# Kernel optimization log

Measured on AMD Instinct MI355X. Metric: run time of the kernel, lower is better.

The kernel has to match this reference:

```python
import math
import jax, jax.numpy as jnp
import numpy as np

B, S, D, H = 2, 2048, 2048, 16
HD = D // H
INV_NORM = 1.0 / math.sqrt(HD)


def _build_alibi(batch, n_heads, seq_len):
    # Standard BLOOM ALiBi slopes (n_heads is a power of two here)
    base = 2.0 ** (-(2.0 ** -(math.log2(n_heads) - 3)))
    slopes = base ** np.arange(1, n_heads + 1, dtype=np.float32)  # [H]
    pos = np.arange(seq_len, dtype=np.float32)  # [S]
    alibi = slopes[:, None] * pos[None, :]  # [H, S]
    alibi = np.broadcast_to(alibi[None], (batch, n_heads, seq_len)).reshape(batch * n_heads, 1, seq_len)
    return jnp.asarray(alibi)


def _build_causal_mask(batch, seq_len):
    neg = jnp.float32(-1e9)
    tril = jnp.tril(jnp.ones((seq_len, seq_len), dtype=bool))
    mask = jnp.where(tril, jnp.float32(0.0), neg)  # [S, S]
    return jnp.broadcast_to(mask[None, None], (batch, 1, seq_len, seq_len))


def setup_inputs() -> dict:
    key = jax.random.key(0)
    ks = jax.random.split(key, 6)
    scale = 0.02
    return {
        "hidden_states": jax.random.normal(ks[0], (B, S, D), jnp.float32),
        "residual": jax.random.normal(ks[1], (B, S, D), jnp.float32),
        "alibi": _build_alibi(B, H, S),
        "attention_mask": _build_causal_mask(B, S),
        "W_qkv": jax.random.normal(ks[2], (3 * D, D), jnp.float32) * scale,
        "b_qkv": jax.random.normal(ks[3], (3 * D,), jnp.float32) * scale,
        "W_dense": jax.random.normal(ks[4], (D, D), jnp.float32) * scale,
        "b_dense": jax.random.normal(ks[5], (D,), jnp.float32) * scale,
    }


def reference(hidden_states, residual, alibi, attention_mask, W_qkv, b_qkv, W_dense, b_dense):
    b, s, d = hidden_states.shape
    # fused QKV projection: [B,S,3D] -> [B,S,H,3,HD]
    fused = (hidden_states @ W_qkv.T + b_qkv).reshape(b, s, H, 3, HD)
    q = fused[..., 0, :].transpose(0, 2, 1, 3)  # [B,H,S,HD]
    k = fused[..., 1, :].transpose(0, 2, 1, 3)
    v = fused[..., 2, :].transpose(0, 2, 1, 3)
    # baddbmm: alibi + inv_norm * q @ k^T ; alibi is [B*H,1,S] -> broadcast over q_len
    scores = alibi.reshape(b, H, 1, s) + INV_NORM * jnp.einsum("bhqd,bhkd->bhqk", q, k)
    scores = scores + attention_mask  # additive causal mask [B,1,S,S]
    probs = jax.nn.softmax(scores.astype(jnp.float32), axis=-1).astype(hidden_states.dtype)
    ctx = jnp.einsum("bhqk,bhkd->bhqd", probs, v)  # [B,H,S,HD]
    ctx = ctx.transpose(0, 2, 1, 3).reshape(b, s, d)  # merge heads
    out = ctx @ W_dense.T + b_dense
    return out + residual  # dropout_add with p=0 (eval)
```

## Files before the change

kernel.cpp:

```cpp
#include <hip/hip_runtime.h>
#include <hip/hip_bf16.h>

typedef __hip_bfloat16 bf16;
typedef __attribute__((ext_vector_type(8))) short s8v;
typedef __attribute__((ext_vector_type(4))) float f4v;

#define B_  2
#define S_  2048
#define D_  2048
#define H_  16
#define HD_ 128
#define INV_NORM 0.08838834764831845f

static __device__ __forceinline__ f4v mfma16(s8v a, s8v b, f4v c) {
    return __builtin_amdgcn_mfma_f32_16x16x32_bf16(a, b, c, 0, 0, 0);
}

static __device__ __forceinline__ void gload_lds(const void* gp, void* lp) {
    __builtin_amdgcn_global_load_lds(
        (const __attribute__((address_space(1))) unsigned int*)gp,
        (__attribute__((address_space(3))) unsigned int*)lp, 16, 0, 0);
}

__global__ __launch_bounds__(256)
void cvt_f32_bf16(const float* __restrict__ src, bf16* __restrict__ dst, int n4)
{
    int i = blockIdx.x * 256 + threadIdx.x;
    if (i < n4) {
        float4 f = ((const float4*)src)[i];
        union { ushort4 u4; bf16 h[4]; } p;
        p.h[0] = __float2bfloat16(f.x);
        p.h[1] = __float2bfloat16(f.y);
        p.h[2] = __float2bfloat16(f.z);
        p.h[3] = __float2bfloat16(f.w);
        ((ushort4*)dst)[i] = p.u4;
    }
}

template <int MODE>
__global__ __launch_bounds__(256)
void gemm_bt(const bf16* __restrict__ A, const bf16* __restrict__ Bw,
             const float* __restrict__ bias, const float* __restrict__ resid,
             bf16* __restrict__ o0, bf16* __restrict__ o1, bf16* __restrict__ o2,
             float* __restrict__ of, int K)
{
    __shared__ __align__(16) bf16 Al[128][32];
    __shared__ __align__(16) bf16 Bl[128][32];
    const int tid  = threadIdx.x;
    const int wave = tid >> 6, lane = tid & 63;
    const int col  = lane & 15, quad = lane >> 4;
    const int wm = (wave >> 1) << 6, wn = (wave & 1) << 6;
    const int bn = blockIdx.x, bm = blockIdx.y;
    const bf16* Ab = A  + (size_t)bm * 128 * K;
    const bf16* Bb = Bw + (size_t)bn * 128 * K;

    const f4v fzero = {0.f, 0.f, 0.f, 0.f};
    f4v acc[4][4];
#pragma unroll
    for (int i = 0; i < 4; i++)
#pragma unroll
        for (int j = 0; j < 4; j++) acc[i][j] = fzero;

    for (int k0 = 0; k0 < K; k0 += 32) {
#pragma unroll
        for (int p = 0; p < 2; p++) {
            const int g = p * 256 + tid;
            const int r = g >> 2, ko = (g & 3) << 3;
            gload_lds(Ab + (size_t)r * K + k0 + ko, (char*)&Al[0][0] + (size_t)g * 16);
            gload_lds(Bb + (size_t)r * K + k0 + ko, (char*)&Bl[0][0] + (size_t)g * 16);
        }
        __syncthreads();
        s8v af[4], bfr[4];
#pragma unroll
        for (int i = 0; i < 4; i++) af[i]  = *(const s8v*)&Al[wm + i * 16 + col][quad * 8];
#pragma unroll
        for (int j = 0; j < 4; j++) bfr[j] = *(const s8v*)&Bl[wn + j * 16 + col][quad * 8];
#pragma unroll
        for (int i = 0; i < 4; i++)
#pragma unroll
            for (int j = 0; j < 4; j++)
                acc[i][j] = mfma16(af[i], bfr[j], acc[i][j]);
        __syncthreads();
    }

    if (MODE == 0) {
        const int t = bn % 3, h = bn / 3;
#pragma unroll
        for (int j = 0; j < 4; j++) {
            const int c = wn + j * 16 + col;
            const float bv = bias[bn * 128 + c];
#pragma unroll
            for (int i = 0; i < 4; i++) {
                const int r  = (bm << 7) + wm + i * 16 + (quad << 2);
                const int bb = r >> 11, s = r & (S_ - 1);
                if (t == 2) {
                    union { ushort4 u4; bf16 hh[4]; } pk;
#pragma unroll
                    for (int rg = 0; rg < 4; rg++)
                        pk.hh[rg] = __float2bfloat16(acc[i][j][rg] + bv);
                    *(ushort4*)(o2 + ((size_t)(bb * H_ + h) * HD_ + c) * S_ + s) = pk.u4;
                } else {
                    bf16* dst = (t == 0) ? o0 : o1;
#pragma unroll
                    for (int rg = 0; rg < 4; rg++)
                        dst[((size_t)(bb * H_ + h) * S_ + (s + rg)) * HD_ + c] =
                            __float2bfloat16(acc[i][j][rg] + bv);
                }
            }
        }
    } else {
#pragma unroll
        for (int j = 0; j < 4; j++) {
            const int c = (bn << 7) + wn + j * 16 + col;
            const float bv = bias[c];
#pragma unroll
            for (int i = 0; i < 4; i++) {
                const int r = (bm << 7) + wm + i * 16 + (quad << 2);
#pragma unroll
                for (int rg = 0; rg < 4; rg++) {
                    const size_t idx = (size_t)(r + rg) * D_ + c;
                    of[idx] = acc[i][j][rg] + bv + resid[idx];
                }
            }
        }
    }
}

#define VMW(s) asm volatile("s_waitcnt " s ::: "memory")
#define BARR() { __builtin_amdgcn_s_barrier(); asm volatile("" ::: "memory"); }

#define RD_A(dst, mibase)                                                       \
  _Pragma("unroll") for (int mi = 0; mi < 4; ++mi) {                            \
    dst[mi][0] = *(const s8v*)(lds + bufB + aR + (mibase + mi) * 4096 + sx0);   \
    dst[mi][1] = *(const s8v*)(lds + bufB + aR + (mibase + mi) * 4096 + sx1);   \
  }
#define RD_B(njbase)                                                            \
  _Pragma("unroll") for (int nj = 0; nj < 2; ++nj) {                            \
    bfr[nj][0] = *(const s8v*)(lds + bufB + bRo + (njbase + nj) * 8192 + sx0);  \
    bfr[nj][1] = *(const s8v*)(lds + bufB + bRo + (njbase + nj) * 8192 + sx1);  \
  }
#define MM(af, mibase, njbase)                                                  \
  __builtin_amdgcn_s_setprio(1);                                                \
  _Pragma("unroll") for (int mi = 0; mi < 4; ++mi)                              \
  _Pragma("unroll") for (int nj = 0; nj < 2; ++nj) {                            \
    acc[mibase + mi][njbase + nj] =                                             \
        mfma16(af[mi][0], bfr[nj][0], acc[mibase + mi][njbase + nj]);           \
    acc[mibase + mi][njbase + nj] =                                             \
        mfma16(af[mi][1], bfr[nj][1], acc[mibase + mi][njbase + nj]);           \
  }                                                                             \
  __builtin_amdgcn_s_setprio(0);

#define KTILE(DOPRE, VA, VB, VC)                                                \
  {                                                                             \
    const int bufB = cur << 16, bufN = (cur ^ 1) << 16;                         \
    const size_t t1 = (size_t)(kt + 1) * 64;                                    \
                          \
    if (DOPRE) { gload_lds(gA + t1 + srcO0, lds + bufN + 0 + dst0);             \
                 gload_lds(gA + t1 + srcO1, lds + bufN + 0 + dst1); }           \
    VMW(VA); BARR();                                                            \
    RD_A(a0, 0); RD_B(0);                                                       \
    MM(a0, 0, 0);                                                               \
                               \
    if (DOPRE) { gload_lds(gB + t1 + srcO0, lds + bufN + 32768 + dst0);         \
                 gload_lds(gB + t1 + srcO1, lds + bufN + 32768 + dst1); }       \
    VMW(VB); BARR();                                                            \
    RD_A(a1, 4);                                                                \
    MM(a1, 4, 0);                                                               \
                               \
    if (DOPRE) { gload_lds(gA2 + t1 + srcO0, lds + bufN + 16384 + dst0);        \
                 gload_lds(gA2 + t1 + srcO1, lds + bufN + 16384 + dst1); }      \
    VMW(VC); BARR();                                                            \
    RD_B(2);                                                                    \
    MM(a0, 0, 2);                                                               \
    BARR();     \
                         \
    if (DOPRE) { gload_lds(gB2 + t1 + srcO0, lds + bufN + 49152 + dst0);        \
                 gload_lds(gB2 + t1 + srcO1, lds + bufN + 49152 + dst1); }      \
    MM(a1, 4, 2);                                                               \
  }

__global__ __launch_bounds__(512, 2)
void gemm_qkv8(const bf16* __restrict__ A, const bf16* __restrict__ Bw,
               const float* __restrict__ bias,
               bf16* __restrict__ o0, bf16* __restrict__ o1, bf16* __restrict__ o2)
{
    __shared__ __align__(16) char lds[131072];
    const int tid  = threadIdx.x;
    const int wave = tid >> 6, lane = tid & 63;
    const int col  = lane & 15, quad = lane >> 4;
    const int wr   = wave >> 2, wc = wave & 3;

    int id = (int)blockIdx.y * 24 + (int)blockIdx.x;
    id = (id & 7) * 48 + (id >> 3);
    const int bm = id / 24, bn = id % 24;

    const bf16* gA  = A  + (size_t)bm * 256 * 2048;
    const bf16* gA2 = gA + (size_t)128 * 2048;
    const bf16* gB  = Bw + (size_t)bn * 256 * 2048;
    const bf16* gB2 = gB + (size_t)128 * 2048;

    const int r0   = tid >> 3, bk0 = tid & 7;
    const int srcO0 = r0 * 2048 + ((bk0 ^ (r0 & 7)) << 3);
    const int srcO1 = srcO0 + 64 * 2048;
    const int dst0 = tid * 16, dst1 = dst0 + 8192;

    const int sx0 = ((quad ^ (col & 7)) << 4);
    const int sx1 = (((4 + quad) ^ (col & 7)) << 4);
    const int aR  = (wr * 16 + col) * 128;
    const int bRo = (wc * 16 + col) * 128 + 32768;

    const f4v fzero = {0.f, 0.f, 0.f, 0.f};
    f4v acc[8][4];
#pragma unroll
    for (int i = 0; i < 8; i++)
#pragma unroll
        for (int j = 0; j < 4; j++) acc[i][j] = fzero;
    s8v a0[4][2], a1[4][2], bfr[2][2];

    gload_lds(gA  + srcO0, lds + 0     + dst0);
    gload_lds(gA  + srcO1, lds + 0     + dst1);
    gload_lds(gB  + srcO0, lds + 32768 + dst0);
    gload_lds(gB  + srcO1, lds + 32768 + dst1);
    gload_lds(gA2 + srcO0, lds + 16384 + dst0);
    gload_lds(gA2 + srcO1, lds + 16384 + dst1);
    gload_lds(gB2 + srcO0, lds + 49152 + dst0);
    gload_lds(gB2 + srcO1, lds + 49152 + dst1);

    int cur = 0;
    for (int kt = 0; kt < 31; ++kt) {
        KTILE(1, "vmcnt(6)", "vmcnt(6)", "vmcnt(6)");
        cur ^= 1;
    }
    {
        const int kt = 31;
        KTILE(0, "vmcnt(4)", "vmcnt(2)", "vmcnt(0)");
    }

#pragma unroll
    for (int mi = 0; mi < 8; ++mi) {
#pragma unroll
        for (int nj = 0; nj < 4; ++nj) {
            const int cg = bn * 2 + (nj >> 1);
            const int t3 = cg % 3, hh = cg / 3;
            const int hd = (nj & 1) * 64 + wc * 16 + col;
            const float bv = bias[cg * 128 + hd];
            const int r = bm * 256 + mi * 32 + wr * 16 + (quad << 2);
            const int bi = r >> 11, srow = r & (S_ - 1);
            if (t3 == 2) {
                union { ushort4 u4; bf16 hv[4]; } pk;
#pragma unroll
                for (int rg = 0; rg < 4; ++rg)
                    pk.hv[rg] = __float2bfloat16(acc[mi][nj][rg] + bv);
                *(ushort4*)(o2 + ((size_t)(bi * H_ + hh) * HD_ + hd) * S_ + srow) = pk.u4;
            } else {
                bf16* dst = (t3 == 0) ? o0 : o1;
#pragma unroll
                for (int rg = 0; rg < 4; ++rg)
                    dst[((size_t)(bi * H_ + hh) * S_ + (srow + rg)) * HD_ + hd] =
                        __float2bfloat16(acc[mi][nj][rg] + bv);
            }
        }
    }
}

__global__ __launch_bounds__(256, 2)
void attn(const bf16* __restrict__ Qb, const bf16* __restrict__ Kb,
          const bf16* __restrict__ Vt, bf16* __restrict__ ctx)
{
    __shared__ __align__(16) char Ksm[2][64 * 256];
    __shared__ __align__(16) char Vsm[2][128 * 128];
    __shared__ __align__(16) char Pl[4 * 16 * 128];

    const int x = blockIdx.x;
    const int bh = blockIdx.y;
    const int u = (bh >> 3) & 1;
    const int qb = u ? x : (int)gridDim.x - 1 - x;
    const int b = bh >> 4, h = bh & 15;
    const int tid = threadIdx.x;
    const int wave = tid >> 6, lane = tid & 63;
    const int col = lane & 15, quad = lane >> 4;
    const int q0 = qb << 6;
    const int qg = q0 + wave * 16 + col;
    const float slope = exp2f(-0.5f * (float)(h + 1));
    const int sw = (col & 7) << 4;

    const bf16* Qp = Qb + ((size_t)bh * S_ + q0 + wave * 16) * HD_;
    s8v aq[4];
#pragma unroll
    for (int c = 0; c < 4; c++)
        aq[c] = *(const s8v*)(Qp + (size_t)col * HD_ + c * 32 + quad * 8);

    const f4v fzero = {0.f, 0.f, 0.f, 0.f};
    f4v o[8];
#pragma unroll
    for (int t = 0; t < 8; t++) o[t] = fzero;
    float m = -1e30f, l = 0.f;

    const bf16* Kbase = Kb + (size_t)bh * S_ * HD_;
    const bf16* Vbase = Vt + (size_t)bh * HD_ * S_;

    int ksrc[4], vsrc[4];
#pragma unroll
    for (int p = 0; p < 4; p++) {
        const int g = p * 256 + tid;
        const int kr = g >> 4, kb = g & 15;
        ksrc[p] = kr * HD_ + ((kb ^ (kr & 7)) << 3);
        const int vr = g >> 3, vb = g & 7;
        vsrc[p] = vr * S_ + ((vb ^ (vr & 7)) << 3);
    }
    const int ldst = tid << 4;

    {
        const bf16* Kp = Kbase;
        const bf16* Vp = Vbase;
#pragma unroll
        for (int p = 0; p < 4; p++) {
            gload_lds(Kp + ksrc[p], Ksm[0] + p * 4096 + ldst);
            gload_lds(Vp + vsrc[p], Vsm[0] + p * 4096 + ldst);
        }
    }
    __syncthreads();

    const int nkt = qb + 1;
    for (int kt = 0; kt < nkt; kt++) {
        const int cur = kt & 1;
        const int k0 = kt << 6;

        if (kt + 1 < nkt) {
            const bf16* Kp = Kbase + (size_t)(kt + 1) * 64 * HD_;
            const bf16* Vp = Vbase + (kt + 1) * 64;
            char* Kd = Ksm[cur ^ 1];
            char* Vd = Vsm[cur ^ 1];
#pragma unroll
            for (int p = 0; p < 4; p++) {
                gload_lds(Kp + ksrc[p], Kd + p * 4096 + ldst);
                gload_lds(Vp + vsrc[p], Vd + p * 4096 + ldst);
            }
        }
        const char* Kcur = Ksm[cur];
        const char* Vcur = Vsm[cur];

        f4v sc[4];
        __builtin_amdgcn_s_setprio(1);
#pragma unroll
        for (int st = 0; st < 4; st++) {
            sc[st] = fzero;
#pragma unroll
            for (int c = 0; c < 4; c++) {
                const s8v kf = *(const s8v*)(Kcur + (st * 16 + col) * 256 +
                                             ((c * 64 + quad * 16) ^ sw));
                sc[st] = mfma16(kf, aq[c], sc[st]);
            }
        }
        __builtin_amdgcn_s_setprio(0);

        float s[16];
        float mx = -1e30f;
#pragma unroll
        for (int st = 0; st < 4; st++)
#pragma unroll
            for (int r = 0; r < 4; r++) {
                const int key = k0 + st * 16 + (quad << 2) + r;
                float v = sc[st][r] * INV_NORM + slope * (float)key;
                v = (key > qg) ? -1e9f : v;
                s[st * 4 + r] = v;
                mx = fmaxf(mx, v);
            }
        mx = fmaxf(mx, __shfl_xor(mx, 16));
        mx = fmaxf(mx, __shfl_xor(mx, 32));
        const float nm = fmaxf(m, mx);
        float ps = 0.f;
#pragma unroll
        for (int i = 0; i < 16; i++) { s[i] = __expf(s[i] - nm); ps += s[i]; }
        ps += __shfl_xor(ps, 16);
        ps += __shfl_xor(ps, 32);
        const float alpha = __expf(m - nm);
        l = l * alpha + ps;
        m = nm;
#pragma unroll
        for (int t = 0; t < 8; t++) o[t] *= alpha;

        char* plw = Pl + wave * 2048 + col * 128;
#pragma unroll
        for (int st = 0; st < 4; st++) {
            union { ushort4 u4; bf16 hh[4]; } pk;
#pragma unroll
            for (int r = 0; r < 4; r++) pk.hh[r] = __float2bfloat16(s[st * 4 + r]);
            *(ushort4*)(plw + ((st * 32 + quad * 8) ^ sw)) = pk.u4;
        }
        const s8v pf0 = *(const s8v*)(plw + ((quad * 16) ^ sw));
        const s8v pf1 = *(const s8v*)(plw + ((64 + quad * 16) ^ sw));

        __builtin_amdgcn_s_setprio(1);
#pragma unroll
        for (int t = 0; t < 8; t++) {
            const s8v vf0 = *(const s8v*)(Vcur + (t * 16 + col) * 128 +
                                          ((quad * 16) ^ sw));
            o[t] = mfma16(vf0, pf0, o[t]);
            const s8v vf1 = *(const s8v*)(Vcur + (t * 16 + col) * 128 +
                                          ((64 + quad * 16) ^ sw));
            o[t] = mfma16(vf1, pf1, o[t]);
        }
        __builtin_amdgcn_s_setprio(0);

        __syncthreads();
    }

    const float rl = 1.0f / l;
#pragma unroll
    for (int t = 0; t < 8; t++) {
        union { ushort4 u4; bf16 hh[4]; } pk;
#pragma unroll
        for (int r = 0; r < 4; r++) pk.hh[r] = __float2bfloat16(o[t][r] * rl);
        *(ushort4*)&ctx[((size_t)(b * S_) + qg) * D_ + h * HD_ + t * 16 + (quad << 2)] =
            pk.u4;
    }
}

extern "C" void kernel_launch(void* const* d_in, const int* in_sizes, int n_in,
                              void* d_out, int out_size, void* d_ws, size_t ws_size,
                              hipStream_t stream)
{
    const float* hs    = (const float*)d_in[0];
    const float* resid = (const float*)d_in[1];
    const float* Wqkv  = (const float*)d_in[4];
    const float* bqkv  = (const float*)d_in[5];
    const float* Wd    = (const float*)d_in[6];
    const float* bd    = (const float*)d_in[7];
    float* out = (float*)d_out;

    const size_t seg  = (size_t)B_ * H_ * S_ * HD_;
    const size_t nHS  = (size_t)B_ * S_ * D_;
    const size_t nWq  = (size_t)3 * D_ * D_;
    const size_t nWd  = (size_t)D_ * D_;
    bf16* Qbuf = (bf16*)d_ws;
    bf16* Kbuf = Qbuf + seg;
    bf16* Vtb  = Kbuf + seg;
    bf16* ctx  = Vtb + seg;
    bf16* hsb  = ctx + seg;
    bf16* Wqb  = hsb + nHS;
    bf16* Wdb  = Wqb + nWq;

    cvt_f32_bf16<<<(int)(nHS / 4 + 255) / 256, 256, 0, stream>>>(hs, hsb, (int)(nHS / 4));
    cvt_f32_bf16<<<(int)(nWq / 4 + 255) / 256, 256, 0, stream>>>(Wqkv, Wqb, (int)(nWq / 4));
    cvt_f32_bf16<<<(int)(nWd / 4 + 255) / 256, 256, 0, stream>>>(Wd, Wdb, (int)(nWd / 4));

    gemm_qkv8<<<dim3(24, 16), 512, 0, stream>>>(hsb, Wqb, bqkv, Qbuf, Kbuf, Vtb);
    attn<<<dim3(32, 32), 256, 0, stream>>>(Qbuf, Kbuf, Vtb, ctx);
    gemm_bt<1><<<dim3(16, 32), 256, 0, stream>>>(ctx, Wdb, bd, resid,
                                                 nullptr, nullptr, nullptr, out, 2048);
}
```

Before: 450.7 us.

## Deepen QKV GEMM LDS prefetch to issue three sub-tiles two k-steps ahead

Restructures the QKV GEMM main loop so that three of the four LDS sub-tiles are prefetched two k-iterations ahead, and the fourth (gB2) one iteration ahead, instead of all four one iteration ahead. Each sub-tile load is issued as soon as its slot in the double buffer is no longer being read, and there is now a single vmcnt wait per k-tile instead of three. The goal is to hide more global-load latency behind MFMA work and cut pipeline stalls. In exchange the prologue, the tail handling and the barrier placement get more complex, and correctness depends on the buffer reuse order being exactly right.

```diff
diff --git a/kernel.cpp b/kernel.cpp
--- a/kernel.cpp
+++ b/kernel.cpp
@@ -150,32 +150,34 @@
   }                                                                             \
   __builtin_amdgcn_s_setprio(0);
 
-#define KTILE(DOPRE, VA, VB, VC)                                                \
+#define STAGE(gptr, t, choff)                                                   \
+  { const size_t co = (size_t)(t) * 64;                                         \
+    gload_lds(gptr + co + srcO0, lds + (((t) & 1) << 16) + (choff) + dst0);     \
+    gload_lds(gptr + co + srcO1, lds + (((t) & 1) << 16) + (choff) + dst1); }
+
+#define KTILE(P0, P2, VA)                                                       \
   {                                                                             \
-    const int bufB = cur << 16, bufN = (cur ^ 1) << 16;                         \
-    const size_t t1 = (size_t)(kt + 1) * 64;                                    \
-                          \
-    if (DOPRE) { gload_lds(gA + t1 + srcO0, lds + bufN + 0 + dst0);             \
-                 gload_lds(gA + t1 + srcO1, lds + bufN + 0 + dst1); }           \
+    const int bufB = (kt & 1) << 16;                                            \
+      \
+      \
     VMW(VA); BARR();                                                            \
+      \
+    if (P0) STAGE(gB2, kt + 1, 49152);                                          \
     RD_A(a0, 0); RD_B(0);                                                       \
     MM(a0, 0, 0);                                                               \
-                               \
-    if (DOPRE) { gload_lds(gB + t1 + srcO0, lds + bufN + 32768 + dst0);         \
-                 gload_lds(gB + t1 + srcO1, lds + bufN + 32768 + dst1); }       \
-    VMW(VB); BARR();                                                            \
+    BARR();                                                                     \
+      \
+    if (P2) STAGE(gA, kt + 2, 0);                                               \
     RD_A(a1, 4);                                                                \
     MM(a1, 4, 0);                                                               \
-                               \
-    if (DOPRE) { gload_lds(gA2 + t1 + srcO0, lds + bufN + 16384 + dst0);        \
-                 gload_lds(gA2 + t1 + srcO1, lds + bufN + 16384 + dst1); }      \
-    VMW(VC); BARR();                                                            \
+    BARR();                                                                     \
+      \
+    if (P2) STAGE(gB, kt + 2, 32768);                                           \
     RD_B(2);                                                                    \
     MM(a0, 0, 2);                                                               \
-    BARR();     \
-                         \
-    if (DOPRE) { gload_lds(gB2 + t1 + srcO0, lds + bufN + 49152 + dst0);        \
-                 gload_lds(gB2 + t1 + srcO1, lds + bufN + 49152 + dst1); }      \
+    BARR();                                                                     \
+      \
+    if (P2) STAGE(gA2, kt + 2, 16384);                                          \
     MM(a1, 4, 2);                                                               \
   }
 
@@ -217,23 +219,22 @@
         for (int j = 0; j < 4; j++) acc[i][j] = fzero;
     s8v a0[4][2], a1[4][2], bfr[2][2];
 
-    gload_lds(gA  + srcO0, lds + 0     + dst0);
-    gload_lds(gA  + srcO1, lds + 0     + dst1);
-    gload_lds(gB  + srcO0, lds + 32768 + dst0);
-    gload_lds(gB  + srcO1, lds + 32768 + dst1);
-    gload_lds(gA2 + srcO0, lds + 16384 + dst0);
-    gload_lds(gA2 + srcO1, lds + 16384 + dst1);
-    gload_lds(gB2 + srcO0, lds + 49152 + dst0);
-    gload_lds(gB2 + srcO1, lds + 49152 + dst1);
-
-    int cur = 0;
-    for (int kt = 0; kt < 31; ++kt) {
-        KTILE(1, "vmcnt(6)", "vmcnt(6)", "vmcnt(6)");
-        cur ^= 1;
-    }
-    {
-        const int kt = 31;
-        KTILE(0, "vmcnt(4)", "vmcnt(2)", "vmcnt(0)");
+    STAGE(gA,  0, 0);
+    STAGE(gB,  0, 32768);
+    STAGE(gA2, 0, 16384);
+    STAGE(gB2, 0, 49152);
+    STAGE(gA,  1, 0);
+    STAGE(gB,  1, 32768);
+    STAGE(gA2, 1, 16384);
+
+    for (int kt = 0; kt < 30; ++kt) {
+        KTILE(1, 1, "vmcnt(6)");
+    }
+    {   const int kt = 30;
+        KTILE(1, 0, "vmcnt(6)");
+    }
+    {   const int kt = 31;
+        KTILE(0, 0, "vmcnt(0)");
     }
 
 #pragma unroll
```

New measurement: 453.1 us. Within noise of the previous version (+0.5%).

## Replace dense output GEMM with pipelined 256x128 tile, swizzled LDS kernel

Applied to the files above, without the earlier changes.

The simple single-buffered 128x128 dense projection GEMM is replaced with an 8-wave kernel that computes 256x128 tiles with double-buffered global-to-LDS loads, XOR-swizzled LDS layout, staggered half-tile prefetch, and a block-id remap for L2 locality. It aims to hide memory latency and raise MFMA utilisation for the output projection plus residual add. The new kernel uses 96KB LDS and a hand-tuned waitcnt schedule, which leaves little margin for pipelining mistakes.

```diff
diff --git a/kernel.cpp b/kernel.cpp
--- a/kernel.cpp
+++ b/kernel.cpp
@@ -34,95 +34,6 @@
         p.h[2] = __float2bfloat16(f.z);
         p.h[3] = __float2bfloat16(f.w);
         ((ushort4*)dst)[i] = p.u4;
-    }
-}
-
-template <int MODE>
-__global__ __launch_bounds__(256)
-void gemm_bt(const bf16* __restrict__ A, const bf16* __restrict__ Bw,
-             const float* __restrict__ bias, const float* __restrict__ resid,
-             bf16* __restrict__ o0, bf16* __restrict__ o1, bf16* __restrict__ o2,
-             float* __restrict__ of, int K)
-{
-    __shared__ __align__(16) bf16 Al[128][32];
-    __shared__ __align__(16) bf16 Bl[128][32];
-    const int tid  = threadIdx.x;
-    const int wave = tid >> 6, lane = tid & 63;
-    const int col  = lane & 15, quad = lane >> 4;
-    const int wm = (wave >> 1) << 6, wn = (wave & 1) << 6;
-    const int bn = blockIdx.x, bm = blockIdx.y;
-    const bf16* Ab = A  + (size_t)bm * 128 * K;
-    const bf16* Bb = Bw + (size_t)bn * 128 * K;
-
-    const f4v fzero = {0.f, 0.f, 0.f, 0.f};
-    f4v acc[4][4];
-#pragma unroll
-    for (int i = 0; i < 4; i++)
-#pragma unroll
-        for (int j = 0; j < 4; j++) acc[i][j] = fzero;
-
-    for (int k0 = 0; k0 < K; k0 += 32) {
-#pragma unroll
-        for (int p = 0; p < 2; p++) {
-            const int g = p * 256 + tid;
-            const int r = g >> 2, ko = (g & 3) << 3;
-            gload_lds(Ab + (size_t)r * K + k0 + ko, (char*)&Al[0][0] + (size_t)g * 16);
-            gload_lds(Bb + (size_t)r * K + k0 + ko, (char*)&Bl[0][0] + (size_t)g * 16);
-        }
-        __syncthreads();
-        s8v af[4], bfr[4];
-#pragma unroll
-        for (int i = 0; i < 4; i++) af[i]  = *(const s8v*)&Al[wm + i * 16 + col][quad * 8];
-#pragma unroll
-        for (int j = 0; j < 4; j++) bfr[j] = *(const s8v*)&Bl[wn + j * 16 + col][quad * 8];
-#pragma unroll
-        for (int i = 0; i < 4; i++)
-#pragma unroll
-            for (int j = 0; j < 4; j++)
-                acc[i][j] = mfma16(af[i], bfr[j], acc[i][j]);
-        __syncthreads();
-    }
-
-    if (MODE == 0) {
-        const int t = bn % 3, h = bn / 3;
-#pragma unroll
-        for (int j = 0; j < 4; j++) {
-            const int c = wn + j * 16 + col;
-            const float bv = bias[bn * 128 + c];
-#pragma unroll
-            for (int i = 0; i < 4; i++) {
-                const int r  = (bm << 7) + wm + i * 16 + (quad << 2);
-                const int bb = r >> 11, s = r & (S_ - 1);
-                if (t == 2) {
-                    union { ushort4 u4; bf16 hh[4]; } pk;
-#pragma unroll
-                    for (int rg = 0; rg < 4; rg++)
-                        pk.hh[rg] = __float2bfloat16(acc[i][j][rg] + bv);
-                    *(ushort4*)(o2 + ((size_t)(bb * H_ + h) * HD_ + c) * S_ + s) = pk.u4;
-                } else {
-                    bf16* dst = (t == 0) ? o0 : o1;
-#pragma unroll
-                    for (int rg = 0; rg < 4; rg++)
-                        dst[((size_t)(bb * H_ + h) * S_ + (s + rg)) * HD_ + c] =
-                            __float2bfloat16(acc[i][j][rg] + bv);
-                }
-            }
-        }
-    } else {
-#pragma unroll
-        for (int j = 0; j < 4; j++) {
-            const int c = (bn << 7) + wn + j * 16 + col;
-            const float bv = bias[c];
-#pragma unroll
-            for (int i = 0; i < 4; i++) {
-                const int r = (bm << 7) + wm + i * 16 + (quad << 2);
-#pragma unroll
-                for (int rg = 0; rg < 4; rg++) {
-                    const size_t idx = (size_t)(r + rg) * D_ + c;
-                    of[idx] = acc[i][j][rg] + bv + resid[idx];
-                }
-            }
-        }
     }
 }
 
@@ -263,6 +174,115 @@
     }
 }
 
+#define STAGE_D(gptr, t, choff)                                                 \
+  { const size_t co = (size_t)(t) * 64;                                         \
+    gload_lds(gptr + co + srcO0, lds + ((t) & 1) * 49152 + (choff) + dst0);     \
+    gload_lds(gptr + co + srcO1, lds + ((t) & 1) * 49152 + (choff) + dst1); }
+
+#define DKTILE(P1, P2, VA)                                                      \
+  {                                                                             \
+    const int bufB = (kt & 1) * 49152;                                          \
+    VMW(VA); BARR();                                                            \
+    if (P1) STAGE_D(gA2, kt + 1, 16384);                                        \
+    _Pragma("unroll") for (int mi = 0; mi < 2; ++mi) {                          \
+      alo[mi][0] = *(const s8v*)(lds + bufB + aR + mi * 8192 + sx0);            \
+      alo[mi][1] = *(const s8v*)(lds + bufB + aR + mi * 8192 + sx1);            \
+    }                                                                           \
+    _Pragma("unroll") for (int nj = 0; nj < 4; ++nj) {                          \
+      bfr[nj][0] = *(const s8v*)(lds + bufB + bR + nj * 4096 + sx0);            \
+      bfr[nj][1] = *(const s8v*)(lds + bufB + bR + nj * 4096 + sx1);            \
+    }                                                                           \
+    __builtin_amdgcn_s_setprio(1);                                              \
+    _Pragma("unroll") for (int mi = 0; mi < 2; ++mi)                            \
+    _Pragma("unroll") for (int nj = 0; nj < 4; ++nj) {                          \
+      acc[mi][nj] = mfma16(alo[mi][0], bfr[nj][0], acc[mi][nj]);                \
+      acc[mi][nj] = mfma16(alo[mi][1], bfr[nj][1], acc[mi][nj]);                \
+    }                                                                           \
+    __builtin_amdgcn_s_setprio(0);                                              \
+    BARR();                                                                     \
+    if (P2) { STAGE_D(gA, kt + 2, 0); STAGE_D(gB, kt + 2, 32768); }             \
+    _Pragma("unroll") for (int mi = 0; mi < 2; ++mi) {                          \
+      ahi[mi][0] = *(const s8v*)(lds + bufB + 16384 + aR + mi * 8192 + sx0);    \
+      ahi[mi][1] = *(const s8v*)(lds + bufB + 16384 + aR + mi * 8192 + sx1);    \
+    }                                                                           \
+    __builtin_amdgcn_s_setprio(1);                                              \
+    _Pragma("unroll") for (int mi = 0; mi < 2; ++mi)                            \
+    _Pragma("unroll") for (int nj = 0; nj < 4; ++nj) {                          \
+      acc[2 + mi][nj] = mfma16(ahi[mi][0], bfr[nj][0], acc[2 + mi][nj]);        \
+      acc[2 + mi][nj] = mfma16(ahi[mi][1], bfr[nj][1], acc[2 + mi][nj]);        \
+    }                                                                           \
+    __builtin_amdgcn_s_setprio(0);                                              \
+  }
+
+__global__ __launch_bounds__(512, 2)
+void gemm_dense8(const bf16* __restrict__ A, const bf16* __restrict__ Bw,
+                 const float* __restrict__ bias, const float* __restrict__ resid,
+                 float* __restrict__ of)
+{
+    __shared__ __align__(16) char lds[98304];
+    const int tid  = threadIdx.x;
+    const int wave = tid >> 6, lane = tid & 63;
+    const int col  = lane & 15, quad = lane >> 4;
+    const int wr   = wave >> 1, wc = wave & 1;
+
+    int id = (int)blockIdx.y * 16 + (int)blockIdx.x;
+    id = (id & 7) * 32 + (id >> 3);
+    const int bm = id >> 4, bn = id & 15;
+
+    const bf16* gA  = A  + (size_t)bm * 256 * 2048;
+    const bf16* gA2 = gA + (size_t)128 * 2048;
+    const bf16* gB  = Bw + (size_t)bn * 128 * 2048;
+
+    const int r0   = tid >> 3, bk0 = tid & 7;
+    const int srcO0 = r0 * 2048 + ((bk0 ^ (r0 & 7)) << 3);
+    const int srcO1 = srcO0 + 64 * 2048;
+    const int dst0 = tid * 16, dst1 = dst0 + 8192;
+
+    const int sx0 = ((quad ^ (col & 7)) << 4);
+    const int sx1 = (((4 + quad) ^ (col & 7)) << 4);
+    const int aR  = (wr * 16 + col) * 128;
+    const int bR  = (wc * 16 + col) * 128 + 32768;
+
+    const f4v fzero = {0.f, 0.f, 0.f, 0.f};
+    f4v acc[4][4];
+#pragma unroll
+    for (int i = 0; i < 4; i++)
+#pragma unroll
+        for (int j = 0; j < 4; j++) acc[i][j] = fzero;
+    s8v alo[2][2], ahi[2][2], bfr[4][2];
+
+    STAGE_D(gA,  0, 0);
+    STAGE_D(gB,  0, 32768);
+    STAGE_D(gA2, 0, 16384);
+    STAGE_D(gA,  1, 0);
+    STAGE_D(gB,  1, 32768);
+
+    for (int kt = 0; kt < 30; ++kt) {
+        DKTILE(1, 1, "vmcnt(4)");
+    }
+    {   const int kt = 30;
+        DKTILE(1, 0, "vmcnt(4)");
+    }
+    {   const int kt = 31;
+        DKTILE(0, 0, "vmcnt(0)");
+    }
+
+#pragma unroll
+    for (int mi = 0; mi < 4; ++mi) {
+#pragma unroll
+        for (int nj = 0; nj < 4; ++nj) {
+            const int c = bn * 128 + nj * 32 + wc * 16 + col;
+            const float bv = bias[c];
+            const int r = bm * 256 + mi * 64 + wr * 16 + (quad << 2);
+#pragma unroll
+            for (int rg = 0; rg < 4; ++rg) {
+                const size_t idx = (size_t)(r + rg) * D_ + c;
+                of[idx] = acc[mi][nj][rg] + bv + resid[idx];
+            }
+        }
+    }
+}
+
 __global__ __launch_bounds__(256, 2)
 void attn(const bf16* __restrict__ Qb, const bf16* __restrict__ Kb,
           const bf16* __restrict__ Vt, bf16* __restrict__ ctx)
@@ -447,6 +467,5 @@
 
     gemm_qkv8<<<dim3(24, 16), 512, 0, stream>>>(hsb, Wqb, bqkv, Qbuf, Kbuf, Vtb);
     attn<<<dim3(32, 32), 256, 0, stream>>>(Qbuf, Kbuf, Vtb, ctx);
-    gemm_bt<1><<<dim3(16, 32), 256, 0, stream>>>(ctx, Wdb, bd, resid,
-                                                 nullptr, nullptr, nullptr, out, 2048);
-}
+    gemm_dense8<<<dim3(16, 16), 512, 0, stream>>>(ctx, Wdb, bd, resid, out);
+}
```

New measurement: 425.0 us. -5.7%, faster.
